# Performance work log

Hardware: AMD Instinct MI355X
Metric: run time of the kernel (lower is better)

## Reference

```python
import jax, jax.numpy as jnp
import numpy as np

B, H, W = 8, 64, 64
EMBED, HEADS, HEAD_DIM = 768, 12, 64
FF = 3072
WS = 14  # window size
SCALE = HEAD_DIM ** -0.5
EPS = 1e-6


def setup_inputs() -> dict:
    key = jax.random.key(0)
    ks = jax.random.split(key, 8)
    def n(k, shp, s=0.02):
        return jax.random.normal(k, shp, jnp.float32) * s
    return {
        "x": jax.random.normal(ks[0], (B, H, W, EMBED), jnp.float32),
        "g1": jnp.ones((EMBED,), jnp.float32),
        "beta1": jnp.zeros((EMBED,), jnp.float32),
        "w_qkv": n(ks[1], (EMBED, 3 * EMBED)),
        "b_qkv": jnp.zeros((3 * EMBED,), jnp.float32),
        "w_proj": n(ks[2], (EMBED, EMBED)),
        "b_proj": jnp.zeros((EMBED,), jnp.float32),
        "rel_pos_h": n(ks[3], (2 * WS - 1, HEAD_DIM)),
        "rel_pos_w": n(ks[4], (2 * WS - 1, HEAD_DIM)),
        "g2": jnp.ones((EMBED,), jnp.float32),
        "beta2": jnp.zeros((EMBED,), jnp.float32),
        "w_fc1": n(ks[5], (EMBED, FF)),
        "b_fc1": jnp.zeros((FF,), jnp.float32),
        "w_fc2": n(ks[6], (FF, EMBED)),
        "b_fc2": jnp.zeros((EMBED,), jnp.float32),
    }


def layer_norm(x, g, b):
    m = jnp.mean(x, axis=-1, keepdims=True)
    v = jnp.mean(jnp.square(x - m), axis=-1, keepdims=True)
    return (x - m) * jax.lax.rsqrt(v + EPS) * g + b


def window_partition(x):
    b, h, w, c = x.shape
    ph, pw = (-h) % WS, (-w) % WS
    x = jnp.pad(x, ((0, 0), (0, ph), (0, pw), (0, 0)))
    hp, wp = h + ph, w + pw
    x = x.reshape(b, hp // WS, WS, wp // WS, WS, c)
    x = x.transpose(0, 1, 3, 2, 4, 5).reshape(-1, WS, WS, c)
    return x, (hp, wp)


def window_unpartition(win, pad_hw, hw):
    hp, wp = pad_hw
    h, w = hw
    b = win.shape[0] // ((hp // WS) * (wp // WS))
    x = win.reshape(b, hp // WS, wp // WS, WS, WS, -1)
    x = x.transpose(0, 1, 3, 2, 4, 5).reshape(b, hp, wp, -1)
    return x[:, :h, :w, :]


def attention(xw, w_qkv, b_qkv, w_proj, b_proj, rel_pos_h, rel_pos_w):
    bw, hs, ws_, c = xw.shape
    n = hs * ws_
    qkv = (xw.reshape(bw, n, c) @ w_qkv + b_qkv).reshape(bw, n, 3, HEADS, HEAD_DIM)
    q, k, v = jnp.moveaxis(qkv, 2, 0)            # each (bw, n, heads, hd)
    q = q.transpose(0, 2, 1, 3)                  # (bw, heads, n, hd)
    k = k.transpose(0, 2, 1, 3)
    v = v.transpose(0, 2, 1, 3)
    attn = jnp.einsum('bhnd,bhmd->bhnm', q * SCALE, k)
    # decomposed relative position bias (q unscaled, per torch reference)
    idx = jnp.arange(WS)[:, None] - jnp.arange(WS)[None, :] + (WS - 1)
    Rh = rel_pos_h[idx]                          # (ws, ws, hd)
    Rw = rel_pos_w[idx]
    r_q = q.reshape(bw, HEADS, WS, WS, HEAD_DIM)
    rel_h = jnp.einsum('bhpqd,pkd->bhpqk', r_q, Rh)
    rel_w = jnp.einsum('bhpqd,qkd->bhpqk', r_q, Rw)
    attn = attn.reshape(bw, HEADS, WS, WS, WS, WS)
    attn = attn + rel_h[..., :, None] + rel_w[..., None, :]
    attn = jax.nn.softmax(attn.reshape(bw, HEADS, n, n), axis=-1)
    out = jnp.einsum('bhnm,bhmd->bhnd', attn, v)
    out = out.transpose(0, 2, 1, 3).reshape(bw, hs, ws_, c)
    return out @ w_proj + b_proj


def reference(x, g1, beta1, w_qkv, b_qkv, w_proj, b_proj, rel_pos_h, rel_pos_w,
              g2, beta2, w_fc1, b_fc1, w_fc2, b_fc2):
    shortcut = x
    h = layer_norm(x, g1, beta1)
    win, pad_hw = window_partition(h)
    a = attention(win, w_qkv, b_qkv, w_proj, b_proj, rel_pos_h, rel_pos_w)
    a = window_unpartition(a, pad_hw, (x.shape[1], x.shape[2]))
    x = shortcut + a
    h2 = layer_norm(x, g2, beta2)
    mlp = jax.nn.gelu(h2 @ w_fc1 + b_fc1, approximate=False) @ w_fc2 + b_fc2
    return x + mlp
```

## Files before the change

### kernel.cpp

```cpp
#include <hip/hip_runtime.h>
#include <cstdint>


typedef unsigned short u16;
typedef __attribute__((ext_vector_type(8))) short short8;
typedef __attribute__((ext_vector_type(4))) float f32x4;

__device__ __forceinline__ u16 f2b(float f) {
    union { float f; unsigned int i; } x; x.f = f;
    unsigned int u = x.i;
    return (u16)((u + 0x7fffu + ((u >> 16) & 1u)) >> 16);
}
__device__ __forceinline__ float b2f(u16 u) {
    union { unsigned int i; float f; } x; x.i = ((unsigned int)u) << 16; return x.f;
}

__device__ __forceinline__ void gload16(const u16* g, u16* l) {
    __builtin_amdgcn_global_load_lds(
        (const __attribute__((address_space(1))) unsigned int*)g,
        (__attribute__((address_space(3))) unsigned int*)l, 16, 0, 0);
}

__device__ __forceinline__ int xcd_swz(int bid, int nwg) {
    int q = nwg >> 3, r = nwg & 7;
    int x = bid & 7, lo = bid >> 3;
    return (x < r ? x * (q + 1) : r * (q + 1) + (x - r) * q) + lo;
}

__global__ __launch_bounds__(256) void transpose_k(
    const float* __restrict__ in, u16* __restrict__ out, int R, int C)
{
    __shared__ float tile[32][33];
    int bpc = C >> 5;
    int r0 = (blockIdx.x / bpc) << 5;
    int c0 = (blockIdx.x % bpc) << 5;
    int lx = threadIdx.x & 31, ly = threadIdx.x >> 5;
#pragma unroll
    for (int s = 0; s < 32; s += 8)
        tile[ly + s][lx] = in[(size_t)(r0 + ly + s) * C + c0 + lx];
    __syncthreads();
#pragma unroll
    for (int s = 0; s < 32; s += 8)
        out[(size_t)(c0 + ly + s) * R + r0 + lx] = f2b(tile[lx][ly + s]);
}

__global__ __launch_bounds__(256) void ln_kernel(
    const float* __restrict__ in, const float* __restrict__ g,
    const float* __restrict__ beta, u16* __restrict__ out, int windowed,
    int row_base)
{
    __shared__ float sbuf[4];
    int tid = threadIdx.x;
    size_t orow = (size_t)blockIdx.x * 768;
    size_t irow;
    if (windowed) {
        int r = row_base + blockIdx.x;
        int win = r / 196, t = r % 196;
        int p = t / 14, q = t % 14;
        int b = win / 25, wt = win % 25;
        int i = (wt / 5) * 14 + p, j = (wt % 5) * 14 + q;
        if (i >= 64 || j >= 64) {
            out[orow + tid] = 0; out[orow + tid + 256] = 0; out[orow + tid + 512] = 0;
            return;
        }
        irow = (((size_t)b * 64 + i) * 64 + j) * 768;
    } else {
        irow = (size_t)blockIdx.x * 768;
    }
    float v0 = in[irow + tid];
    float v1 = in[irow + tid + 256];
    float v2 = in[irow + tid + 512];
    float s = v0 + v1 + v2;
#pragma unroll
    for (int off = 32; off; off >>= 1) s += __shfl_xor(s, off, 64);
    if ((tid & 63) == 0) sbuf[tid >> 6] = s;
    __syncthreads();
    float mean = (sbuf[0] + sbuf[1] + sbuf[2] + sbuf[3]) * (1.f / 768.f);
    __syncthreads();
    float d0 = v0 - mean, d1 = v1 - mean, d2 = v2 - mean;
    float sq = d0 * d0 + d1 * d1 + d2 * d2;
#pragma unroll
    for (int off = 32; off; off >>= 1) sq += __shfl_xor(sq, off, 64);
    if ((tid & 63) == 0) sbuf[tid >> 6] = sq;
    __syncthreads();
    float var = (sbuf[0] + sbuf[1] + sbuf[2] + sbuf[3]) * (1.f / 768.f);
    float rs = rsqrtf(var + 1e-6f);
    out[orow + tid]       = f2b(d0 * rs * g[tid]       + beta[tid]);
    out[orow + tid + 256] = f2b(d1 * rs * g[tid + 256] + beta[tid + 256]);
    out[orow + tid + 512] = f2b(d2 * rs * g[tid + 512] + beta[tid + 512]);
}

#define BM 128
#define BN 128
#define BK 32

template <int EPI>
__global__ __launch_bounds__(256) void gemm_bt(
    const u16* __restrict__ A, const u16* __restrict__ Bt,
    const float* __restrict__ bias, void* __restrict__ CoutV,
    const float* __restrict__ resid, int M, int N, int K, int row_base)
{
    __shared__ __align__(16) u16 As[BM * BK];
    __shared__ __align__(16) u16 Bs[BN * BK];
    const int tid = threadIdx.x;
    const int lane = tid & 63, wave = tid >> 6;
    const int wr = wave >> 1, wc = wave & 1;
    const int quad = lane >> 4, l16 = lane & 15;
    const int ntile = N / BN;
    const int swz = xcd_swz(blockIdx.x, gridDim.x);
    const int m0 = (swz / ntile) * BM;
    const int n0 = (swz % ntile) * BN;

    f32x4 acc[4][4] = {};

    const int t0 = wave * 2;
    const size_t arow0 = (size_t)(m0 + t0 * 16 + (lane >> 2)) * K + (lane & 3) * 8;
    const size_t arow1 = arow0 + (size_t)16 * K;
    const size_t brow0 = (size_t)(n0 + t0 * 16 + (lane >> 2)) * K + (lane & 3) * 8;
    const size_t brow1 = brow0 + (size_t)16 * K;
    u16* lA0 = As + t0 * 16 * BK;
    u16* lA1 = As + (t0 + 1) * 16 * BK;
    u16* lB0 = Bs + t0 * 16 * BK;
    u16* lB1 = Bs + (t0 + 1) * 16 * BK;

    for (int k0 = 0; k0 < K; k0 += BK) {
        __syncthreads();
        gload16(A + arow0 + k0, lA0);
        gload16(A + arow1 + k0, lA1);
        gload16(Bt + brow0 + k0, lB0);
        gload16(Bt + brow1 + k0, lB1);
        __syncthreads();
        short8 af[4], bfr[4];
#pragma unroll
        for (int i = 0; i < 4; i++)
            af[i] = *(const short8*)(As + (wr * 64 + i * 16 + l16) * BK + quad * 8);
#pragma unroll
        for (int i = 0; i < 4; i++)
            bfr[i] = *(const short8*)(Bs + (wc * 64 + i * 16 + l16) * BK + quad * 8);
        __builtin_amdgcn_s_setprio(1);
#pragma unroll
        for (int mi = 0; mi < 4; mi++)
#pragma unroll
            for (int ni = 0; ni < 4; ni++)
                acc[mi][ni] = __builtin_amdgcn_mfma_f32_16x16x32_bf16(
                    af[mi], bfr[ni], acc[mi][ni], 0, 0, 0);
        __builtin_amdgcn_s_setprio(0);
    }

#pragma unroll
    for (int mi = 0; mi < 4; mi++) {
#pragma unroll
        for (int ni = 0; ni < 4; ni++) {
            const int gn = n0 + wc * 64 + ni * 16 + l16;
            const float bv = bias[gn];
#pragma unroll
            for (int r = 0; r < 4; r++) {
                const int row = m0 + wr * 64 + mi * 16 + quad * 4 + r;
                if (row >= M) continue;
                float v = acc[mi][ni][r] + bv;
                if (EPI == 0) {
                    ((u16*)CoutV)[(size_t)row * N + gn] = f2b(v);
                } else if (EPI == 1) {
                    int grow = row_base + row;
                    int win = grow / 196, t = grow % 196;
                    int p = t / 14, q = t % 14;
                    int b = win / 25, wt = win % 25;
                    int i = (wt / 5) * 14 + p, j = (wt % 5) * 14 + q;
                    if (i < 64 && j < 64) {
                        size_t idx = (((size_t)b * 64 + i) * 64 + j) * 768 + gn;
                        ((float*)CoutV)[idx] = resid[idx] + v;
                    }
                } else if (EPI == 2) {
                    float gl = 0.5f * v * (1.0f + erff(v * 0.70710678118654752f));
                    ((u16*)CoutV)[(size_t)row * N + gn] = f2b(gl);
                } else {
                    size_t idx = (size_t)(row_base + row) * 768 + gn;
                    ((float*)CoutV)[idx] = resid[idx] + v;
                }
            }
        }
    }
}

#define AT_W 72
#define PB_W 40

__global__ __launch_bounds__(256) void attn_mfma(
    const u16* __restrict__ qkv,
    const float* __restrict__ relh, const float* __restrict__ relw,
    u16* __restrict__ out)
{
    __shared__ __align__(16) u16 pbuf[4][32 * PB_W];
    __shared__ __align__(16) u16 Kc[64 * AT_W];
    __shared__ __align__(16) u16 Vt[64 * AT_W];
    u16* rel_ext = &pbuf[0][0];

    const int nwg = gridDim.x;
    const int swzb = xcd_swz(blockIdx.x, nwg);
    const int win = swzb / 24, rem = swzb % 24;
    const int head = rem >> 1, half = rem & 1;
    const int row0 = half * 128;
    const int tid = threadIdx.x, lane = tid & 63, wave = tid >> 6;
    const int quad = lane >> 4, l16 = lane & 15;
    const size_t base = (size_t)win * 196 * 2304 + (size_t)head * 64;

    short8 qf[2][2];
#pragma unroll
    for (int mi = 0; mi < 2; mi++) {
        int tok = row0 + wave * 32 + mi * 16 + l16;
        int rt = tok < 196 ? tok : 195;
        const u16* qp = qkv + base + (size_t)rt * 2304 + quad * 8;
        qf[mi][0] = *(const short8*)(qp);
        qf[mi][1] = *(const short8*)(qp + 32);
    }

    for (int e = tid; e < 64 * 64; e += 256) {
        int rr = e >> 6, cc = e & 63;
        float v = 0.f;
        if (rr < 27)      v = 8.f * relh[rr * 64 + cc];
        else if (rr < 54) v = 8.f * relw[(rr - 27) * 64 + cc];
        Kc[rr * AT_W + cc] = f2b(v);
    }
    if (tid < 128) {
        u16* rp = rel_ext + tid * 32;
        uint4 z = make_uint4(0u, 0u, 0u, 0u);
        *(uint4*)(rp) = z; *(uint4*)(rp + 8) = z;
        *(uint4*)(rp + 16) = z; *(uint4*)(rp + 24) = z;
        rp[31] = f2b(-1e30f);
    }
    __syncthreads();

#pragma unroll
    for (int cb = 0; cb < 2; cb++) {
#pragma unroll
        for (int nt = 0; nt < 2; nt++) {
            const u16* kp_ = Kc + (cb * 32 + nt * 16 + l16) * AT_W + quad * 8;
            short8 b0 = *(const short8*)(kp_);
            short8 b1 = *(const short8*)(kp_ + 32);
            int i = cb * 32 + nt * 16 + l16;
#pragma unroll
            for (int mi = 0; mi < 2; mi++) {
                f32x4 c = {};
                c = __builtin_amdgcn_mfma_f32_16x16x32_bf16(qf[mi][0], b0, c, 0, 0, 0);
                c = __builtin_amdgcn_mfma_f32_16x16x32_bf16(qf[mi][1], b1, c, 0, 0, 0);
#pragma unroll
                for (int r = 0; r < 4; r++) {
                    int row = wave * 32 + mi * 16 + quad * 4 + r;
                    int grow = row0 + row;
                    int rowB = grow < 196 ? grow : 195;
                    int p = rowB / 14, qq = rowB % 14;
                    if (i < 27) {
                        int t = p + 13 - i;
                        if (t >= 0 && t < 14) rel_ext[row * 32 + t] = f2b(c[r]);
                    } else if (i < 54) {
                        int t = qq + 13 - (i - 27);
                        if (t >= 0 && t < 14) rel_ext[row * 32 + 14 + t] = f2b(c[r]);
                    }
                }
            }
        }
    }
    short8 qe[2];
#pragma unroll
    for (int mi = 0; mi < 2; mi++)
        qe[mi] = *(const short8*)(rel_ext + (wave * 32 + mi * 16 + l16) * 32 + quad * 8);

    f32x4 acc[2][4] = {};
    float ml_[2][4], ll_[2][4];
#pragma unroll
    for (int mi = 0; mi < 2; mi++)
#pragma unroll
        for (int r = 0; r < 4; r++) { ml_[mi][r] = -1e30f; ll_[mi][r] = 0.f; }

#pragma unroll 1
    for (int c = 0; c < 4; c++) {
        const int kbase = c * 64;
        __syncthreads();
        {
            int key = tid >> 2;
            int cg  = (tid & 3) << 4;
            int gk = kbase + key;
            uint4 k0 = make_uint4(0u,0u,0u,0u), k1 = k0, v0 = k0, v1 = k0;
            if (gk < 196) {
                const u16* kp_ = qkv + base + 768  + (size_t)gk * 2304 + cg;
                const u16* vp_ = qkv + base + 1536 + (size_t)gk * 2304 + cg;
                k0 = *(const uint4*)(kp_); k1 = *(const uint4*)(kp_ + 8);
                v0 = *(const uint4*)(vp_); v1 = *(const uint4*)(vp_ + 8);
            }
            *(uint4*)(Kc + key * AT_W + cg)     = k0;
            *(uint4*)(Kc + key * AT_W + cg + 8) = k1;
            union { uint4 u; u16 h[8]; } a, b; a.u = v0; b.u = v1;
#pragma unroll
            for (int i = 0; i < 8; i++) Vt[(cg + i) * AT_W + key] = a.h[i];
#pragma unroll
            for (int i = 0; i < 8; i++) Vt[(cg + 8 + i) * AT_W + key] = b.h[i];
        }
        __syncthreads();

        short8 bo[4];
        {
            const u16 one = 0x3F80;
#pragma unroll
            for (int nt = 0; nt < 4; nt++) {
                int key = kbase + nt * 16 + l16;
                int inval = key >= 196;
                int kp = key / 14, kq = key - kp * 14;
                union { short8 s; u16 h[8]; } u;
#pragma unroll
                for (int j = 0; j < 8; j++) {
                    int t = quad * 8 + j;
                    u16 v = 0;
                    if (!inval && t == kp) v = one;
                    if (!inval && t >= 14 && (t - 14) == kq) v = one;
                    if (inval && t == 31) v = one;
                    u.h[j] = v;
                }
                bo[nt] = u.s;
            }
        }

        f32x4 s23[2][2];
#pragma unroll
        for (int mi = 0; mi < 2; mi++) {
            f32x4 s[4];
            __builtin_amdgcn_s_setprio(1);
#pragma unroll
            for (int nt = 0; nt < 4; nt++) {
                const u16* kp_ = Kc + (nt * 16 + l16) * AT_W + quad * 8;
                short8 kf0 = *(const short8*)(kp_);
                short8 kf1 = *(const short8*)(kp_ + 32);
                f32x4 t = {};
                t = __builtin_amdgcn_mfma_f32_16x16x32_bf16(qf[mi][0], kf0, t, 0, 0, 0);
                t = __builtin_amdgcn_mfma_f32_16x16x32_bf16(qf[mi][1], kf1, t, 0, 0, 0);
                t = __builtin_amdgcn_mfma_f32_16x16x32_bf16(qe[mi],    bo[nt], t, 0, 0, 0);
                s[nt] = t * 0.125f;
            }
            __builtin_amdgcn_s_setprio(0);
#pragma unroll
            for (int r = 0; r < 4; r++) {
                float mx = fmaxf(fmaxf(s[0][r], s[1][r]), fmaxf(s[2][r], s[3][r]));
#pragma unroll
                for (int off = 8; off; off >>= 1) mx = fmaxf(mx, __shfl_xor(mx, off, 16));
                float mo = ml_[mi][r];
                float mn = fmaxf(mo, mx);
                float alpha = __expf(mo - mn);
                ml_[mi][r] = mn;
                float p0 = __expf(s[0][r] - mn), p1 = __expf(s[1][r] - mn);
                float p2 = __expf(s[2][r] - mn), p3 = __expf(s[3][r] - mn);
                float ps = (p0 + p1) + (p2 + p3);
#pragma unroll
                for (int off = 8; off; off >>= 1) ps += __shfl_xor(ps, off, 16);
                ll_[mi][r] = ll_[mi][r] * alpha + ps;
#pragma unroll
                for (int ni = 0; ni < 4; ni++) acc[mi][ni][r] *= alpha;
                s[0][r] = p0; s[1][r] = p1; s[2][r] = p2; s[3][r] = p3;
            }
#pragma unroll
            for (int nt = 0; nt < 2; nt++)
#pragma unroll
                for (int r = 0; r < 4; r++)
                    pbuf[wave][(mi * 16 + quad * 4 + r) * PB_W + nt * 16 + l16] = f2b(s[nt][r]);
            s23[mi][0] = s[2]; s23[mi][1] = s[3];
        }

        __builtin_amdgcn_s_setprio(1);
#pragma unroll
        for (int mi = 0; mi < 2; mi++) {
            short8 pf = *(const short8*)(pbuf[wave] + (mi * 16 + l16) * PB_W + quad * 8);
#pragma unroll
            for (int ni = 0; ni < 4; ni++) {
                short8 vfn = *(const short8*)(Vt + (ni * 16 + l16) * AT_W + quad * 8);
                acc[mi][ni] = __builtin_amdgcn_mfma_f32_16x16x32_bf16(pf, vfn, acc[mi][ni], 0, 0, 0);
            }
        }
        __builtin_amdgcn_s_setprio(0);
#pragma unroll
        for (int mi = 0; mi < 2; mi++)
#pragma unroll
            for (int h = 0; h < 2; h++)
#pragma unroll
                for (int r = 0; r < 4; r++)
                    pbuf[wave][(mi * 16 + quad * 4 + r) * PB_W + h * 16 + l16] = f2b(s23[mi][h][r]);
        __builtin_amdgcn_s_setprio(1);
#pragma unroll
        for (int mi = 0; mi < 2; mi++) {
            short8 pf = *(const short8*)(pbuf[wave] + (mi * 16 + l16) * PB_W + quad * 8);
#pragma unroll
            for (int ni = 0; ni < 4; ni++) {
                short8 vfn = *(const short8*)(Vt + (ni * 16 + l16) * AT_W + 32 + quad * 8);
                acc[mi][ni] = __builtin_amdgcn_mfma_f32_16x16x32_bf16(pf, vfn, acc[mi][ni], 0, 0, 0);
            }
        }
        __builtin_amdgcn_s_setprio(0);
    }

#pragma unroll
    for (int mi = 0; mi < 2; mi++)
#pragma unroll
        for (int r = 0; r < 4; r++) {
            int tok = row0 + wave * 32 + mi * 16 + quad * 4 + r;
            if (tok < 196) {
                float inv = 1.f / ll_[mi][r];
                size_t ob = (size_t)(win * 196 + tok) * 768 + head * 64;
#pragma unroll
                for (int ni = 0; ni < 4; ni++)
                    out[ob + ni * 16 + l16] = f2b(acc[mi][ni][r] * inv);
            }
        }
}

extern "C" void kernel_launch(void* const* d_in, const int* in_sizes, int n_in,
                              void* d_out, int out_size, void* d_ws, size_t ws_size,
                              hipStream_t stream)
{
    const float* x      = (const float*)d_in[0];
    const float* g1     = (const float*)d_in[1];
    const float* beta1  = (const float*)d_in[2];
    const float* w_qkv  = (const float*)d_in[3];
    const float* b_qkv  = (const float*)d_in[4];
    const float* w_proj = (const float*)d_in[5];
    const float* b_proj = (const float*)d_in[6];
    const float* rph    = (const float*)d_in[7];
    const float* rpw    = (const float*)d_in[8];
    const float* g2     = (const float*)d_in[9];
    const float* beta2  = (const float*)d_in[10];
    const float* w_fc1  = (const float*)d_in[11];
    const float* b_fc1  = (const float*)d_in[12];
    const float* w_fc2  = (const float*)d_in[13];
    const float* b_fc2  = (const float*)d_in[14];
    float* out = (float*)d_out;

    const size_t WT = 14155776;
    size_t b1 = 0, b2 = 0;
    int nc = 0, mc = 0;
    auto fits = [&](int a, int m) -> bool {
        size_t rows = (size_t)(200 / a) * 196, toks = (size_t)32768 / m;
        size_t bb1 = rows * 768 * 2 >= toks * 768 * 2 ? rows * 768 * 2 : toks * 768 * 2;
        size_t bb2 = rows * 2304 * 2 >= toks * 3072 * 2 ? rows * 2304 * 2 : toks * 3072 * 2;
        if (WT + bb1 + bb2 <= ws_size) { b1 = bb1; b2 = bb2; nc = a; mc = m; return true; }
        return false;
    };
    if (!fits(1, 1) && !fits(1, 2) && !fits(2, 2) && !fits(2, 4) && !fits(4, 4))
        return;

    char* ws = (char*)d_ws;
    u16* wt0 = (u16*)ws;
    u16* wt1 = wt0 + 2304 * 768;
    u16* wt2 = wt1 + 768 * 768;
    u16* wt3 = wt2 + 3072 * 768;
    u16* buf1 = (u16*)(ws + WT);
    u16* buf2 = (u16*)(ws + WT + b1);

    dim3 blk(256);

    transpose_k<<<(768/32)*(2304/32), blk, 0, stream>>>(w_qkv,  wt0, 768, 2304);
    transpose_k<<<(768/32)*(768/32),  blk, 0, stream>>>(w_proj, wt1, 768, 768);
    transpose_k<<<(768/32)*(3072/32), blk, 0, stream>>>(w_fc1,  wt2, 768, 3072);
    transpose_k<<<(3072/32)*(768/32), blk, 0, stream>>>(w_fc2,  wt3, 3072, 768);

    {
        const int nw = 200 / nc, rows = nw * 196;
        const int mt = (rows + 127) / 128;
        for (int c = 0; c < nc; c++) {
            const int rb = c * rows;
            ln_kernel<<<rows, blk, 0, stream>>>(x, g1, beta1, buf1, 1, rb);
            gemm_bt<0><<<dim3(mt * (2304/128)), blk, 0, stream>>>(
                buf1, wt0, b_qkv, buf2, nullptr, rows, 2304, 768, 0);
            attn_mfma<<<nw * 24, blk, 0, stream>>>(buf2, rph, rpw, buf1);
            gemm_bt<1><<<dim3(mt * (768/128)), blk, 0, stream>>>(
                buf1, wt1, b_proj, out, x, rows, 768, 768, rb);
        }
    }

    {
        const int tk = 32768 / mc;
        const int mt2 = tk / 128;
        for (int c = 0; c < mc; c++) {
            const int rb = c * tk;
            ln_kernel<<<tk, blk, 0, stream>>>(
                out + (size_t)rb * 768, g2, beta2, buf1, 0, 0);
            gemm_bt<2><<<dim3(mt2 * (3072/128)), blk, 0, stream>>>(
                buf1, wt2, b_fc1, buf2, nullptr, tk, 3072, 768, 0);
            gemm_bt<3><<<dim3(mt2 * (768/128)), blk, 0, stream>>>(
                buf2, wt3, b_fc2, out, out, tk, 768, 3072, rb);
        }
    }
}
```

Measured before the change: 1.446 ms.

## Replace 128x128 GEMM with double-buffered 256x256x64 swizzled-LDS MFMA kernel

The GEMM kernel is rebuilt to use 256x256 output tiles with a K step of 64 and 512 threads. LDS is double-buffered so the async global-to-LDS loads for the next K slice overlap the MFMAs on the current one, with explicit vmcnt waits. An XOR swizzle on the LDS layout avoids bank conflicts, and the fragment loads are ordered so A and B fragments are reused across quadrants. The larger tiles raise arithmetic intensity but need about 128KB of LDS, leaving one block per CU. They also make wave quantization worse for the narrow N=768 GEMMs and read padded rows past M.

```diff
diff --git a/kernel.cpp b/kernel.cpp
--- a/kernel.cpp
+++ b/kernel.cpp
@@ -90,72 +90,160 @@
     out[orow + tid + 512] = f2b(d2 * rs * g[tid + 512] + beta[tid + 512]);
 }
 
-#define BM 128
-#define BN 128
-#define BK 32
+#define GBM 256
+#define GBN 256
+#define GBK 64
+
+__device__ __forceinline__ short8 lds_frag(const u16* base, int row, int ks,
+                                           int quad, int l7) {
+    return *(const short8*)(base + row * 64 + ((((ks << 2) + quad) ^ l7) << 3));
+}
 
 template <int EPI>
-__global__ __launch_bounds__(256) void gemm_bt(
+__global__ __launch_bounds__(512) void gemm256(
     const u16* __restrict__ A, const u16* __restrict__ Bt,
     const float* __restrict__ bias, void* __restrict__ CoutV,
     const float* __restrict__ resid, int M, int N, int K, int row_base)
 {
-    __shared__ __align__(16) u16 As[BM * BK];
-    __shared__ __align__(16) u16 Bs[BN * BK];
+    __shared__ __align__(16) u16 LdsA[2][GBM * GBK];
+    __shared__ __align__(16) u16 LdsB[2][GBN * GBK];
     const int tid = threadIdx.x;
     const int lane = tid & 63, wave = tid >> 6;
-    const int wr = wave >> 1, wc = wave & 1;
-    const int quad = lane >> 4, l16 = lane & 15;
-    const int ntile = N / BN;
+    const int wr = wave >> 2, wc = wave & 3;
+    const int quad = lane >> 4, l16 = lane & 15, l7 = lane & 7;
+    const int ntile = N / GBN;
     const int swz = xcd_swz(blockIdx.x, gridDim.x);
-    const int m0 = (swz / ntile) * BM;
-    const int n0 = (swz % ntile) * BN;
-
-    f32x4 acc[4][4] = {};
-
-    const int t0 = wave * 2;
-    const size_t arow0 = (size_t)(m0 + t0 * 16 + (lane >> 2)) * K + (lane & 3) * 8;
-    const size_t arow1 = arow0 + (size_t)16 * K;
-    const size_t brow0 = (size_t)(n0 + t0 * 16 + (lane >> 2)) * K + (lane & 3) * 8;
-    const size_t brow1 = brow0 + (size_t)16 * K;
-    u16* lA0 = As + t0 * 16 * BK;
-    u16* lA1 = As + (t0 + 1) * 16 * BK;
-    u16* lB0 = Bs + t0 * 16 * BK;
-    u16* lB1 = Bs + (t0 + 1) * 16 * BK;
-
-    for (int k0 = 0; k0 < K; k0 += BK) {
-        __syncthreads();
-        gload16(A + arow0 + k0, lA0);
-        gload16(A + arow1 + k0, lA1);
-        gload16(Bt + brow0 + k0, lB0);
-        gload16(Bt + brow1 + k0, lB1);
-        __syncthreads();
-        short8 af[4], bfr[4];
-#pragma unroll
-        for (int i = 0; i < 4; i++)
-            af[i] = *(const short8*)(As + (wr * 64 + i * 16 + l16) * BK + quad * 8);
-#pragma unroll
-        for (int i = 0; i < 4; i++)
-            bfr[i] = *(const short8*)(Bs + (wc * 64 + i * 16 + l16) * BK + quad * 8);
+    const int m0 = (swz / ntile) * GBM;
+    const int n0 = (swz % ntile) * GBN;
+
+    const int rl = lane >> 3;
+    const int cl = ((lane & 7) ^ rl) << 3;
+    const int sA = wave * 4;
+    int aoff[4], boff[4];
+    int lA[4], lB[4];
+#pragma unroll
+    for (int q = 0; q < 4; q++) {
+        aoff[q] = (m0 + (sA + q) * 8 + rl) * K + cl;
+        boff[q] = (n0 + (sA + q) * 8 + rl) * K + cl;
+        lA[q] = (sA + q) * 512;
+        lB[q] = (sA + q) * 512;
+    }
+
+    f32x4 acc[8][4] = {};
+    const int nt = K / GBK;
+
+#pragma unroll
+    for (int q = 0; q < 4; q++) {
+        gload16(A + aoff[q],  &LdsA[0][lA[q]]);
+        gload16(Bt + boff[q], &LdsB[0][lB[q]]);
+    }
+
+#pragma unroll 1
+    for (int g = 0; g < nt; ++g) {
+        const int cur = g & 1;
+        __builtin_amdgcn_sched_barrier(0);
+        __builtin_amdgcn_s_barrier();
+        __builtin_amdgcn_sched_barrier(0);
+        if (g + 1 < nt) {
+            const int koff = (g + 1) * GBK;
+            const int nboff = (cur ^ 1) * (GBM * GBK);
+#pragma unroll
+            for (int q = 0; q < 4; q++) {
+                gload16(A + aoff[q] + koff,  &LdsA[0][nboff + lA[q]]);
+                gload16(Bt + boff[q] + koff, &LdsB[0][nboff + lB[q]]);
+            }
+            __builtin_amdgcn_sched_barrier(0);
+            asm volatile("s_waitcnt vmcnt(8)" ::: "memory");
+        } else {
+            asm volatile("s_waitcnt vmcnt(0)" ::: "memory");
+        }
+        __builtin_amdgcn_sched_barrier(0);
+        __builtin_amdgcn_s_barrier();
+        __builtin_amdgcn_sched_barrier(0);
+
+        const u16* Ab = &LdsA[cur][0];
+        const u16* Bb = &LdsB[cur][0];
+        short8 a[4][2], b[2][2];
+
+#pragma unroll
+        for (int m = 0; m < 4; m++)
+#pragma unroll
+            for (int ks = 0; ks < 2; ks++)
+                a[m][ks] = lds_frag(Ab, wr * 128 + m * 16 + l16, ks, quad, l7);
+#pragma unroll
+        for (int n = 0; n < 2; n++)
+#pragma unroll
+            for (int ks = 0; ks < 2; ks++)
+                b[n][ks] = lds_frag(Bb, wc * 64 + n * 16 + l16, ks, quad, l7);
         __builtin_amdgcn_s_setprio(1);
 #pragma unroll
-        for (int mi = 0; mi < 4; mi++)
-#pragma unroll
-            for (int ni = 0; ni < 4; ni++)
-                acc[mi][ni] = __builtin_amdgcn_mfma_f32_16x16x32_bf16(
-                    af[mi], bfr[ni], acc[mi][ni], 0, 0, 0);
+        for (int m = 0; m < 4; m++)
+#pragma unroll
+            for (int n = 0; n < 2; n++)
+#pragma unroll
+                for (int ks = 0; ks < 2; ks++)
+                    acc[m][n] = __builtin_amdgcn_mfma_f32_16x16x32_bf16(
+                        a[m][ks], b[n][ks], acc[m][n], 0, 0, 0);
         __builtin_amdgcn_s_setprio(0);
-    }
-
-#pragma unroll
-    for (int mi = 0; mi < 4; mi++) {
+
+#pragma unroll
+        for (int n = 0; n < 2; n++)
+#pragma unroll
+            for (int ks = 0; ks < 2; ks++)
+                b[n][ks] = lds_frag(Bb, wc * 64 + 32 + n * 16 + l16, ks, quad, l7);
+        __builtin_amdgcn_s_setprio(1);
+#pragma unroll
+        for (int m = 0; m < 4; m++)
+#pragma unroll
+            for (int n = 0; n < 2; n++)
+#pragma unroll
+                for (int ks = 0; ks < 2; ks++)
+                    acc[m][2 + n] = __builtin_amdgcn_mfma_f32_16x16x32_bf16(
+                        a[m][ks], b[n][ks], acc[m][2 + n], 0, 0, 0);
+        __builtin_amdgcn_s_setprio(0);
+
+#pragma unroll
+        for (int m = 0; m < 4; m++)
+#pragma unroll
+            for (int ks = 0; ks < 2; ks++)
+                a[m][ks] = lds_frag(Ab, wr * 128 + 64 + m * 16 + l16, ks, quad, l7);
+        __builtin_amdgcn_s_setprio(1);
+#pragma unroll
+        for (int m = 0; m < 4; m++)
+#pragma unroll
+            for (int n = 0; n < 2; n++)
+#pragma unroll
+                for (int ks = 0; ks < 2; ks++)
+                    acc[4 + m][2 + n] = __builtin_amdgcn_mfma_f32_16x16x32_bf16(
+                        a[m][ks], b[n][ks], acc[4 + m][2 + n], 0, 0, 0);
+        __builtin_amdgcn_s_setprio(0);
+
+#pragma unroll
+        for (int n = 0; n < 2; n++)
+#pragma unroll
+            for (int ks = 0; ks < 2; ks++)
+                b[n][ks] = lds_frag(Bb, wc * 64 + n * 16 + l16, ks, quad, l7);
+        __builtin_amdgcn_s_setprio(1);
+#pragma unroll
+        for (int m = 0; m < 4; m++)
+#pragma unroll
+            for (int n = 0; n < 2; n++)
+#pragma unroll
+                for (int ks = 0; ks < 2; ks++)
+                    acc[4 + m][n] = __builtin_amdgcn_mfma_f32_16x16x32_bf16(
+                        a[m][ks], b[n][ks], acc[4 + m][n], 0, 0, 0);
+        __builtin_amdgcn_s_setprio(0);
+    }
+
+#pragma unroll
+    for (int mi = 0; mi < 8; mi++) {
 #pragma unroll
         for (int ni = 0; ni < 4; ni++) {
             const int gn = n0 + wc * 64 + ni * 16 + l16;
             const float bv = bias[gn];
 #pragma unroll
             for (int r = 0; r < 4; r++) {
-                const int row = m0 + wr * 64 + mi * 16 + quad * 4 + r;
+                const int row = m0 + wr * 128 + mi * 16 + quad * 4 + r;
                 if (row >= M) continue;
                 float v = acc[mi][ni][r] + bv;
                 if (EPI == 0) {
@@ -164,10 +252,10 @@
                     int grow = row_base + row;
                     int win = grow / 196, t = grow % 196;
                     int p = t / 14, q = t % 14;
-                    int b = win / 25, wt = win % 25;
+                    int b_ = win / 25, wt = win % 25;
                     int i = (wt / 5) * 14 + p, j = (wt % 5) * 14 + q;
                     if (i < 64 && j < 64) {
-                        size_t idx = (((size_t)b * 64 + i) * 64 + j) * 768 + gn;
+                        size_t idx = (((size_t)b_ * 64 + i) * 64 + j) * 768 + gn;
                         ((float*)CoutV)[idx] = resid[idx] + v;
                     }
                 } else if (EPI == 2) {
@@ -451,7 +539,7 @@
     u16* buf1 = (u16*)(ws + WT);
     u16* buf2 = (u16*)(ws + WT + b1);
 
-    dim3 blk(256);
+    dim3 blk(256), blk5(512);
 
     transpose_k<<<(768/32)*(2304/32), blk, 0, stream>>>(w_qkv,  wt0, 768, 2304);
     transpose_k<<<(768/32)*(768/32),  blk, 0, stream>>>(w_proj, wt1, 768, 768);
@@ -460,28 +548,28 @@
 
     {
         const int nw = 200 / nc, rows = nw * 196;
-        const int mt = (rows + 127) / 128;
+        const int mt = (rows + 255) / 256;
         for (int c = 0; c < nc; c++) {
             const int rb = c * rows;
             ln_kernel<<<rows, blk, 0, stream>>>(x, g1, beta1, buf1, 1, rb);
-            gemm_bt<0><<<dim3(mt * (2304/128)), blk, 0, stream>>>(
+            gemm256<0><<<dim3(mt * (2304/256)), blk5, 0, stream>>>(
                 buf1, wt0, b_qkv, buf2, nullptr, rows, 2304, 768, 0);
             attn_mfma<<<nw * 24, blk, 0, stream>>>(buf2, rph, rpw, buf1);
-            gemm_bt<1><<<dim3(mt * (768/128)), blk, 0, stream>>>(
+            gemm256<1><<<dim3(mt * (768/256)), blk5, 0, stream>>>(
                 buf1, wt1, b_proj, out, x, rows, 768, 768, rb);
         }
     }
 
     {
         const int tk = 32768 / mc;
-        const int mt2 = tk / 128;
+        const int mt2 = (tk + 255) / 256;
         for (int c = 0; c < mc; c++) {
             const int rb = c * tk;
             ln_kernel<<<tk, blk, 0, stream>>>(
                 out + (size_t)rb * 768, g2, beta2, buf1, 0, 0);
-            gemm_bt<2><<<dim3(mt2 * (3072/128)), blk, 0, stream>>>(
+            gemm256<2><<<dim3(mt2 * (3072/256)), blk5, 0, stream>>>(
                 buf1, wt2, b_fc1, buf2, nullptr, tk, 3072, 768, 0);
-            gemm_bt<3><<<dim3(mt2 * (768/128)), blk, 0, stream>>>(
+            gemm256<3><<<dim3(mt2 * (768/256)), blk5, 0, stream>>>(
                 buf2, wt3, b_fc2, out, out, tk, 768, 3072, rb);
         }
     }
```

Measured after the change: 1.610 ms. 11.3% more time.

## Double-buffer GEMM LDS tiles with BK=64 and XOR-swizzled layout

Applied to the files above, without the earlier changes.

Replaces the single-buffered BK=32 GEMM with a ping-pong pipeline over two 128x64 LDS buffers per operand. The next K-slice is prefetched via global_load_lds while MFMAs run on the current one, gated by explicit vmcnt waits and barriers. LDS columns are XOR-swizzled by row to avoid bank conflicts on the fragment reads. This uses 64KB of LDS per block, which can reduce occupancy, and with nth = K>>7 it assumes K is a multiple of 128.

```diff
diff --git a/kernel.cpp b/kernel.cpp
--- a/kernel.cpp
+++ b/kernel.cpp
@@ -90,61 +90,115 @@
     out[orow + tid + 512] = f2b(d2 * rs * g[tid + 512] + beta[tid + 512]);
 }
 
-#define BM 128
-#define BN 128
-#define BK 32
+
+__device__ __forceinline__ void compute_tile(
+    const u16* Ab, const u16* Bb, f32x4 (&acc)[4][4],
+    int wr, int wc, int quad, int l16, int l7)
+{
+    short8 a_[4][2], b_[4][2];
+#pragma unroll
+    for (int m = 0; m < 4; m++)
+#pragma unroll
+        for (int ks = 0; ks < 2; ks++)
+            a_[m][ks] = *(const short8*)(Ab + (wr * 64 + m * 16 + l16) * 64
+                                            + ((((ks << 2) + quad) ^ l7) << 3));
+#pragma unroll
+    for (int n = 0; n < 4; n++)
+#pragma unroll
+        for (int ks = 0; ks < 2; ks++)
+            b_[n][ks] = *(const short8*)(Bb + (wc * 64 + n * 16 + l16) * 64
+                                            + ((((ks << 2) + quad) ^ l7) << 3));
+    __builtin_amdgcn_s_setprio(1);
+#pragma unroll
+    for (int m = 0; m < 4; m++)
+#pragma unroll
+        for (int n = 0; n < 4; n++)
+#pragma unroll
+            for (int ks = 0; ks < 2; ks++)
+                acc[m][n] = __builtin_amdgcn_mfma_f32_16x16x32_bf16(
+                    a_[m][ks], b_[n][ks], acc[m][n], 0, 0, 0);
+    __builtin_amdgcn_s_setprio(0);
+}
 
 template <int EPI>
-__global__ __launch_bounds__(256) void gemm_bt(
+__global__ __launch_bounds__(256) void gemm128(
     const u16* __restrict__ A, const u16* __restrict__ Bt,
     const float* __restrict__ bias, void* __restrict__ CoutV,
     const float* __restrict__ resid, int M, int N, int K, int row_base)
 {
-    __shared__ __align__(16) u16 As[BM * BK];
-    __shared__ __align__(16) u16 Bs[BN * BK];
+    __shared__ __align__(16) u16 As0[128 * 64];
+    __shared__ __align__(16) u16 As1[128 * 64];
+    __shared__ __align__(16) u16 Bs0[128 * 64];
+    __shared__ __align__(16) u16 Bs1[128 * 64];
+
     const int tid = threadIdx.x;
     const int lane = tid & 63, wave = tid >> 6;
     const int wr = wave >> 1, wc = wave & 1;
-    const int quad = lane >> 4, l16 = lane & 15;
-    const int ntile = N / BN;
+    const int quad = lane >> 4, l16 = lane & 15, l7 = lane & 7;
+    const int ntile = N / 128;
     const int swz = xcd_swz(blockIdx.x, gridDim.x);
-    const int m0 = (swz / ntile) * BM;
-    const int n0 = (swz % ntile) * BN;
+    const int m0 = (swz / ntile) * 128;
+    const int n0 = (swz % ntile) * 128;
+
+    const int rl = lane >> 3;
+    const int cl = ((lane & 7) ^ rl) << 3;
+    int aoff[4], boff[4];
+#pragma unroll
+    for (int q = 0; q < 4; q++) {
+        aoff[q] = (m0 + wave * 32 + q * 8 + rl) * K + cl;
+        boff[q] = (n0 + wave * 32 + q * 8 + rl) * K + cl;
+    }
+    const int lws = wave * 32 * 64;
 
     f32x4 acc[4][4] = {};
-
-    const int t0 = wave * 2;
-    const size_t arow0 = (size_t)(m0 + t0 * 16 + (lane >> 2)) * K + (lane & 3) * 8;
-    const size_t arow1 = arow0 + (size_t)16 * K;
-    const size_t brow0 = (size_t)(n0 + t0 * 16 + (lane >> 2)) * K + (lane & 3) * 8;
-    const size_t brow1 = brow0 + (size_t)16 * K;
-    u16* lA0 = As + t0 * 16 * BK;
-    u16* lA1 = As + (t0 + 1) * 16 * BK;
-    u16* lB0 = Bs + t0 * 16 * BK;
-    u16* lB1 = Bs + (t0 + 1) * 16 * BK;
-
-    for (int k0 = 0; k0 < K; k0 += BK) {
-        __syncthreads();
-        gload16(A + arow0 + k0, lA0);
-        gload16(A + arow1 + k0, lA1);
-        gload16(Bt + brow0 + k0, lB0);
-        gload16(Bt + brow1 + k0, lB1);
-        __syncthreads();
-        short8 af[4], bfr[4];
-#pragma unroll
-        for (int i = 0; i < 4; i++)
-            af[i] = *(const short8*)(As + (wr * 64 + i * 16 + l16) * BK + quad * 8);
-#pragma unroll
-        for (int i = 0; i < 4; i++)
-            bfr[i] = *(const short8*)(Bs + (wc * 64 + i * 16 + l16) * BK + quad * 8);
-        __builtin_amdgcn_s_setprio(1);
-#pragma unroll
-        for (int mi = 0; mi < 4; mi++)
-#pragma unroll
-            for (int ni = 0; ni < 4; ni++)
-                acc[mi][ni] = __builtin_amdgcn_mfma_f32_16x16x32_bf16(
-                    af[mi], bfr[ni], acc[mi][ni], 0, 0, 0);
-        __builtin_amdgcn_s_setprio(0);
+    const int nth = K >> 7;
+
+#pragma unroll
+    for (int q = 0; q < 4; q++) {
+        gload16(A  + aoff[q], As0 + lws + q * 512);
+        gload16(Bt + boff[q], Bs0 + lws + q * 512);
+    }
+
+#pragma unroll 1
+    for (int it = 0; it < nth; ++it) {
+        __builtin_amdgcn_sched_barrier(0);
+        __builtin_amdgcn_s_barrier();
+        __builtin_amdgcn_sched_barrier(0);
+        {
+            const int k1 = (2 * it + 1) << 6;
+#pragma unroll
+            for (int q = 0; q < 4; q++) {
+                gload16(A  + aoff[q] + k1, As1 + lws + q * 512);
+                gload16(Bt + boff[q] + k1, Bs1 + lws + q * 512);
+            }
+        }
+        __builtin_amdgcn_sched_barrier(0);
+        asm volatile("s_waitcnt vmcnt(8)" ::: "memory");
+        __builtin_amdgcn_sched_barrier(0);
+        __builtin_amdgcn_s_barrier();
+        __builtin_amdgcn_sched_barrier(0);
+        compute_tile(As0, Bs0, acc, wr, wc, quad, l16, l7);
+
+        __builtin_amdgcn_sched_barrier(0);
+        __builtin_amdgcn_s_barrier();
+        __builtin_amdgcn_sched_barrier(0);
+        if (it + 1 < nth) {
+            const int k2 = (2 * it + 2) << 6;
+#pragma unroll
+            for (int q = 0; q < 4; q++) {
+                gload16(A  + aoff[q] + k2, As0 + lws + q * 512);
+                gload16(Bt + boff[q] + k2, Bs0 + lws + q * 512);
+            }
+            __builtin_amdgcn_sched_barrier(0);
+            asm volatile("s_waitcnt vmcnt(8)" ::: "memory");
+        } else {
+            __builtin_amdgcn_sched_barrier(0);
+            asm volatile("s_waitcnt vmcnt(0)" ::: "memory");
+        }
+        __builtin_amdgcn_sched_barrier(0);
+        __builtin_amdgcn_s_barrier();
+        __builtin_amdgcn_sched_barrier(0);
+        compute_tile(As1, Bs1, acc, wr, wc, quad, l16, l7);
     }
 
 #pragma unroll
@@ -164,10 +218,10 @@
                     int grow = row_base + row;
                     int win = grow / 196, t = grow % 196;
                     int p = t / 14, q = t % 14;
-                    int b = win / 25, wt = win % 25;
+                    int b_ = win / 25, wt = win % 25;
                     int i = (wt / 5) * 14 + p, j = (wt % 5) * 14 + q;
                     if (i < 64 && j < 64) {
-                        size_t idx = (((size_t)b * 64 + i) * 64 + j) * 768 + gn;
+                        size_t idx = (((size_t)b_ * 64 + i) * 64 + j) * 768 + gn;
                         ((float*)CoutV)[idx] = resid[idx] + v;
                     }
                 } else if (EPI == 2) {
@@ -464,10 +518,10 @@
         for (int c = 0; c < nc; c++) {
             const int rb = c * rows;
             ln_kernel<<<rows, blk, 0, stream>>>(x, g1, beta1, buf1, 1, rb);
-            gemm_bt<0><<<dim3(mt * (2304/128)), blk, 0, stream>>>(
+            gemm128<0><<<dim3(mt * (2304/128)), blk, 0, stream>>>(
                 buf1, wt0, b_qkv, buf2, nullptr, rows, 2304, 768, 0);
             attn_mfma<<<nw * 24, blk, 0, stream>>>(buf2, rph, rpw, buf1);
-            gemm_bt<1><<<dim3(mt * (768/128)), blk, 0, stream>>>(
+            gemm128<1><<<dim3(mt * (768/128)), blk, 0, stream>>>(
                 buf1, wt1, b_proj, out, x, rows, 768, 768, rb);
         }
     }
@@ -479,9 +533,9 @@
             const int rb = c * tk;
             ln_kernel<<<tk, blk, 0, stream>>>(
                 out + (size_t)rb * 768, g2, beta2, buf1, 0, 0);
-            gemm_bt<2><<<dim3(mt2 * (3072/128)), blk, 0, stream>>>(
+            gemm128<2><<<dim3(mt2 * (3072/128)), blk, 0, stream>>>(
                 buf1, wt2, b_fc1, buf2, nullptr, tk, 3072, 768, 0);
-            gemm_bt<3><<<dim3(mt2 * (768/128)), blk, 0, stream>>>(
+            gemm128<3><<<dim3(mt2 * (768/128)), blk, 0, stream>>>(
                 buf2, wt3, b_fc2, out, out, tk, 768, 3072, rb);
         }
     }
```

After: 1.545 ms. 1.07x slower.

## Double GEMM K-tile to 64 with XOR-swizzled LDS layout

Applied to the files above, without the earlier changes.

Raises the GEMM K tile from 32 to 64, so each main-loop iteration loads twice as much data and runs two MFMA sub-steps. This halves the number of barrier pairs per K sweep. The LDS tile is stored with an XOR swizzle on 16-byte column chunks (row index within the 8-row group) so that the 128-byte-stride rows do not cause bank conflicts on the fragment reads. LDS use doubles to 32 KB per block, which may lower occupancy, and there is still no double buffering.

```diff
diff --git a/kernel.cpp b/kernel.cpp
--- a/kernel.cpp
+++ b/kernel.cpp
@@ -92,7 +92,7 @@
 
 #define BM 128
 #define BN 128
-#define BK 32
+#define BK 64
 
 template <int EPI>
 __global__ __launch_bounds__(256) void gemm_bt(
@@ -106,6 +106,7 @@
     const int lane = tid & 63, wave = tid >> 6;
     const int wr = wave >> 1, wc = wave & 1;
     const int quad = lane >> 4, l16 = lane & 15;
+    const int l7 = lane & 7;
     const int ntile = N / BN;
     const int swz = xcd_swz(blockIdx.x, gridDim.x);
     const int m0 = (swz / ntile) * BM;
@@ -113,38 +114,43 @@
 
     f32x4 acc[4][4] = {};
 
-    const int t0 = wave * 2;
-    const size_t arow0 = (size_t)(m0 + t0 * 16 + (lane >> 2)) * K + (lane & 3) * 8;
-    const size_t arow1 = arow0 + (size_t)16 * K;
-    const size_t brow0 = (size_t)(n0 + t0 * 16 + (lane >> 2)) * K + (lane & 3) * 8;
-    const size_t brow1 = brow0 + (size_t)16 * K;
-    u16* lA0 = As + t0 * 16 * BK;
-    u16* lA1 = As + (t0 + 1) * 16 * BK;
-    u16* lB0 = Bs + t0 * 16 * BK;
-    u16* lB1 = Bs + (t0 + 1) * 16 * BK;
+    const int rl = lane >> 3;
+    const int cl = ((lane & 7) ^ rl) << 3;
+    size_t aoff[4], boff[4];
+#pragma unroll
+    for (int q = 0; q < 4; q++) {
+        aoff[q] = (size_t)(m0 + wave * 32 + q * 8 + rl) * K + cl;
+        boff[q] = (size_t)(n0 + wave * 32 + q * 8 + rl) * K + cl;
+    }
+    const int lws = wave * 2048;
 
     for (int k0 = 0; k0 < K; k0 += BK) {
         __syncthreads();
-        gload16(A + arow0 + k0, lA0);
-        gload16(A + arow1 + k0, lA1);
-        gload16(Bt + brow0 + k0, lB0);
-        gload16(Bt + brow1 + k0, lB1);
+#pragma unroll
+        for (int q = 0; q < 4; q++) {
+            gload16(A  + aoff[q] + k0, As + lws + q * 512);
+            gload16(Bt + boff[q] + k0, Bs + lws + q * 512);
+        }
         __syncthreads();
-        short8 af[4], bfr[4];
-#pragma unroll
-        for (int i = 0; i < 4; i++)
-            af[i] = *(const short8*)(As + (wr * 64 + i * 16 + l16) * BK + quad * 8);
-#pragma unroll
-        for (int i = 0; i < 4; i++)
-            bfr[i] = *(const short8*)(Bs + (wc * 64 + i * 16 + l16) * BK + quad * 8);
-        __builtin_amdgcn_s_setprio(1);
-#pragma unroll
-        for (int mi = 0; mi < 4; mi++)
-#pragma unroll
-            for (int ni = 0; ni < 4; ni++)
-                acc[mi][ni] = __builtin_amdgcn_mfma_f32_16x16x32_bf16(
-                    af[mi], bfr[ni], acc[mi][ni], 0, 0, 0);
-        __builtin_amdgcn_s_setprio(0);
+#pragma unroll
+        for (int ks = 0; ks < 2; ks++) {
+            short8 af[4], bfr[4];
+            const int rsw = (((ks << 2) + quad) ^ l7) << 3;
+#pragma unroll
+            for (int i = 0; i < 4; i++)
+                af[i] = *(const short8*)(As + (wr * 64 + i * 16 + l16) * 64 + rsw);
+#pragma unroll
+            for (int i = 0; i < 4; i++)
+                bfr[i] = *(const short8*)(Bs + (wc * 64 + i * 16 + l16) * 64 + rsw);
+            __builtin_amdgcn_s_setprio(1);
+#pragma unroll
+            for (int mi = 0; mi < 4; mi++)
+#pragma unroll
+                for (int ni = 0; ni < 4; ni++)
+                    acc[mi][ni] = __builtin_amdgcn_mfma_f32_16x16x32_bf16(
+                        af[mi], bfr[ni], acc[mi][ni], 0, 0, 0);
+            __builtin_amdgcn_s_setprio(0);
+        }
     }
 
 #pragma unroll
```

New measurement: 1.341 ms. 7.3% less time.
